# Optimization experiments

Measured on AMD Instinct MI355X. Metric: run time of the kernel, lower is better.

## Reference

```python
import jax, jax.numpy as jnp
import numpy as np

EPS = 1e-4  # clamp floor used by the torch module

def setup_inputs() -> dict:
    key = jax.random.key(0)
    k1, k2, k3, k4, k5 = jax.random.split(key, 5)
    B, C, T, BOT = 32, 1536, 2000, 128
    x = jax.random.normal(k1, (B, C, T), dtype=jnp.float32)
    W1 = jax.random.normal(k2, (BOT, 3 * C), dtype=jnp.float32) * 0.02
    b1 = jax.random.normal(k3, (BOT,), dtype=jnp.float32) * 0.02
    W2 = jax.random.normal(k4, (C, BOT), dtype=jnp.float32) * 0.02
    b2 = jax.random.normal(k5, (C,), dtype=jnp.float32) * 0.02
    return {"x": x, "W1": W1, "b1": b1, "W2": W2, "b2": b2}

def reference(x, W1, b1, W2, b2):
    # x: [B, C, T]
    T = x.shape[-1]
    mean = jnp.mean(x, axis=2, keepdims=True)                       # [B,C,1]
    var = jnp.var(x, axis=2, keepdims=True, ddof=1)                 # torch.var is unbiased
    std = jnp.sqrt(jnp.clip(var, EPS, None))                        # [B,C,1]
    glob = jnp.concatenate(
        [x,
         jnp.broadcast_to(mean, x.shape),
         jnp.broadcast_to(std, x.shape)], axis=1)                   # [B,3C,T]
    # conv1x1 -> relu -> conv1x1 over channel dim
    h = jnp.einsum('oc,bct->bot', W1, glob) + b1[None, :, None]     # [B,BOT,T]
    h = jax.nn.relu(h)
    w = jnp.einsum('ob,bkt->bot'.replace('bkt','xkt').replace('bot','xot'), W2, h)  # placeholder avoided
    w = jnp.einsum('cb,xbt->xct', W2, h) + b2[None, :, None]        # [B,C,T]
    w = jax.nn.softmax(w, axis=2)                                   # softmax over time
    wmean = jnp.sum(x * w, axis=2)                                  # [B,C]
    wsd = jnp.sqrt(jnp.clip(jnp.sum(x * x * w, axis=2) - wmean ** 2, EPS, None))
    return jnp.concatenate([wmean, wsd], axis=1)                    # [B,2C]
```

## Files before the change

kernel.cpp:

```cpp
#include <hip/hip_runtime.h>
#include <hip/hip_bf16.h>
#include <math.h>
#include <float.h>

#define B_    32
#define C_    1536
#define T_    2000
#define TP_   2048
#define BOT_  128
#define EPS_  1e-4f

#define CH    64
#define NCH   24
#define TC    128
#define NTS   16
#define NT_ST 8

typedef __attribute__((ext_vector_type(8))) short short8;
typedef __attribute__((ext_vector_type(4))) short short4v;
typedef __attribute__((ext_vector_type(4))) float f32x4;

static __device__ __forceinline__ unsigned short f2bf(float f) {
    unsigned u = __float_as_uint(f);
    u += 0x7FFFu + ((u >> 16) & 1u);
    return (unsigned short)(u >> 16);
}
static __device__ __forceinline__ float bf2f(unsigned short u) {
    return __uint_as_float(((unsigned)u) << 16);
}

__global__ __launch_bounds__(256) void stats_transpose(
    const float* __restrict__ x, float* __restrict__ spart,
    unsigned short* __restrict__ xt) {
    const int cb0 = blockIdx.x * 64;
    const int tc  = blockIdx.y;
    const int b   = blockIdx.z;
    const int tid = threadIdx.x;
    const int crow = tid >> 4;
    const int t4   = tid & 15;

    __shared__ __align__(16) unsigned short Tl[64 * 72];

    const float* xb = x + ((size_t)b * C_ + cb0) * T_;
    unsigned short* xo = xt + (size_t)b * TP_ * C_ + cb0;

    float s1[4] = {0.f, 0.f, 0.f, 0.f}, s2[4] = {0.f, 0.f, 0.f, 0.f};

    const int tt0 = tc * 256;
    for (int tt = tt0; tt < tt0 + 256; tt += 64) {
        __syncthreads();
        const int tg = tt + t4 * 4;
        #pragma unroll
        for (int i = 0; i < 4; ++i) {
            const int c = crow + 16 * i;
            f32x4 v;
            if (tg < T_) {
                v = *reinterpret_cast<const f32x4*>(xb + (size_t)c * T_ + tg);
            } else {
                v = (f32x4){0.f, 0.f, 0.f, 0.f};
            }
            s1[i] += (v[0] + v[1]) + (v[2] + v[3]);
            s2[i] = fmaf(v[0], v[0], fmaf(v[1], v[1],
                    fmaf(v[2], v[2], fmaf(v[3], v[3], s2[i]))));
            #pragma unroll
            for (int j = 0; j < 4; ++j)
                Tl[(t4 * 4 + j) * 72 + c] = f2bf(v[j]);
        }
        __syncthreads();
        #pragma unroll
        for (int jj = 0; jj < 2; ++jj) {
            int idx = tid + 256 * jj;
            int t = idx >> 3, c8 = idx & 7;
            short8 vv = *reinterpret_cast<const short8*>(&Tl[t * 72 + c8 * 8]);
            *reinterpret_cast<short8*>(xo + (size_t)(tt + t) * C_ + c8 * 8) = vv;
        }
    }

    #pragma unroll
    for (int i = 0; i < 4; ++i) {
        #pragma unroll
        for (int off = 1; off < 16; off <<= 1) {
            s1[i] += __shfl_xor(s1[i], off);
            s2[i] += __shfl_xor(s2[i], off);
        }
    }
    if (t4 == 0) {
        float* sp = spart + ((size_t)(b * NT_ST + tc) * 2) * C_ + cb0;
        #pragma unroll
        for (int i = 0; i < 4; ++i) {
            const int c = crow + 16 * i;
            sp[c]      = s1[i];
            sp[C_ + c] = s2[i];
        }
    }
}

__global__ __launch_bounds__(256) void cvt_kernel(
    const float* __restrict__ W1, const float* __restrict__ W2,
    unsigned short* __restrict__ W1b, unsigned short* __restrict__ W2b) {
    int idx = blockIdx.x * 256 + threadIdx.x;
    if (idx < BOT_ * C_) {
        int o = idx / C_, c = idx - o * C_;
        W1b[idx] = f2bf(W1[(size_t)o * (3 * C_) + c]);
        W2b[idx] = f2bf(W2[idx]);
    }
}

__global__ __launch_bounds__(256) void cb_kernel(
    const float* __restrict__ W1, const float* __restrict__ b1,
    const float* __restrict__ spart, float* __restrict__ cb) {
    __shared__ __align__(16) float ml[C_];
    __shared__ __align__(16) float sl[C_];
    const int b = blockIdx.x, tid = threadIdx.x;

    for (int c = tid; c < C_; c += 256) {
        float s1 = 0.f, s2 = 0.f;
        #pragma unroll
        for (int tc = 0; tc < NT_ST; ++tc) {
            const float* sp = spart + ((size_t)(b * NT_ST + tc) * 2) * C_ + c;
            s1 += sp[0];
            s2 += sp[C_];
        }
        float mean = s1 / (float)T_;
        float var  = (s2 - s1 * mean) / (float)(T_ - 1);
        ml[c] = mean;
        sl[c] = sqrtf(fmaxf(var, EPS_));
    }
    __syncthreads();

    const int grp = tid >> 4, j = tid & 15;
    #pragma unroll
    for (int p = 0; p < 8; ++p) {
        const int o = p * 16 + grp;
        const float* wm = W1 + (size_t)o * (3 * C_) + C_;
        const float* ws = wm + C_;
        float am = 0.f, as = 0.f;
        #pragma unroll 4
        for (int k = 0; k < 24; ++k) {
            const int c = k * 64 + j * 4;
            float4 wmv = *reinterpret_cast<const float4*>(wm + c);
            float4 wsv = *reinterpret_cast<const float4*>(ws + c);
            float4 mlv = *reinterpret_cast<const float4*>(&ml[c]);
            float4 slv = *reinterpret_cast<const float4*>(&sl[c]);
            am = fmaf(wmv.x, mlv.x, fmaf(wmv.y, mlv.y,
                 fmaf(wmv.z, mlv.z, fmaf(wmv.w, mlv.w, am))));
            as = fmaf(wsv.x, slv.x, fmaf(wsv.y, slv.y,
                 fmaf(wsv.z, slv.z, fmaf(wsv.w, slv.w, as))));
        }
        float v = am + as;
        v += __shfl_xor(v, 1); v += __shfl_xor(v, 2);
        v += __shfl_xor(v, 4); v += __shfl_xor(v, 8);
        if (j == 0) cb[(size_t)b * BOT_ + o] = b1[o] + v;
    }
}

typedef const __attribute__((address_space(1))) unsigned int* gas_ptr;
typedef __attribute__((address_space(3))) unsigned int* las_ptr;

__global__ __launch_bounds__(512) void fused_main(
    const unsigned short* __restrict__ xt,
    const unsigned short* __restrict__ W1b, const unsigned short* __restrict__ W2b,
    const float* __restrict__ cb, float* __restrict__ part) {
    const int b   = blockIdx.y;
    const int ts  = blockIdx.x;
    const int t0  = ts * TC;
    const int tid = threadIdx.x;
    const int lane = tid & 63;
    const int w   = tid >> 6;
    const int oh  = w >> 2, th = w & 3;
    const int g   = lane >> 4, li = lane & 15;

    __shared__ __align__(16) unsigned short LDS[4 * 8192];
    unsigned short* Hl = LDS;

    const unsigned short* xtb = xt + (size_t)b * TP_ * C_;

    f32x4 hacc[4][2];
    #pragma unroll
    for (int mi = 0; mi < 4; ++mi)
        #pragma unroll
        for (int ni = 0; ni < 2; ++ni)
            hacc[mi][ni] = (f32x4){0.f, 0.f, 0.f, 0.f};

    const unsigned short* gX[2];
    const unsigned short* gW[2];
    #pragma unroll
    for (int i = 0; i < 2; ++i) {
        int s = i * 512 + tid;
        int r = s >> 3, sl = s & 7;
        gX[i] = xtb + (size_t)(t0 + r) * C_ + ((sl ^ (r & 7)) * 8);
        gW[i] = W1b + (size_t)r * C_ + ((sl ^ (r & 7)) * 8);
    }

    auto STAGE = [&](int p, int kc) {
        unsigned short* bx = LDS + p * 16384;
        unsigned short* bw = bx + 8192;
        #pragma unroll
        for (int i = 0; i < 2; ++i)
            __builtin_amdgcn_global_load_lds(
                (gas_ptr)(gX[i] + kc), (las_ptr)&bx[(i * 512 + w * 64) * 8], 16, 0, 0);
        #pragma unroll
        for (int i = 0; i < 2; ++i)
            __builtin_amdgcn_global_load_lds(
                (gas_ptr)(gW[i] + kc), (las_ptr)&bw[(i * 512 + w * 64) * 8], 16, 0, 0);
    };

    auto COMPUTE = [&](int p) {
        const unsigned short* bx = LDS + p * 16384;
        const unsigned short* bw = bx + 8192;
        __builtin_amdgcn_s_setprio(1);
        #pragma unroll
        for (int ks = 0; ks < 2; ++ks) {
            short8 a[4], bb4[2];
            #pragma unroll
            for (int mi = 0; mi < 4; ++mi) {
                int o = oh * 64 + mi * 16 + li;
                a[mi] = *reinterpret_cast<const short8*>(
                    &bw[o * 64 + (((ks * 4 + g) ^ (o & 7)) << 3)]);
            }
            #pragma unroll
            for (int ni = 0; ni < 2; ++ni) {
                int t = th * 32 + ni * 16 + li;
                bb4[ni] = *reinterpret_cast<const short8*>(
                    &bx[t * 64 + (((ks * 4 + g) ^ (t & 7)) << 3)]);
            }
            #pragma unroll
            for (int mi = 0; mi < 4; ++mi)
                #pragma unroll
                for (int ni = 0; ni < 2; ++ni)
                    hacc[mi][ni] = __builtin_amdgcn_mfma_f32_16x16x32_bf16(a[mi], bb4[ni], hacc[mi][ni], 0, 0, 0);
        }
        __builtin_amdgcn_s_setprio(0);
    };

    STAGE(0, 0);
    STAGE(1, CH);

    for (int k = 0; k < NCH - 1; ++k) {
        const int cur = k & 1;
        asm volatile("s_waitcnt vmcnt(4)" ::: "memory");
        __builtin_amdgcn_s_barrier();
        COMPUTE(cur);
        __builtin_amdgcn_s_barrier();
        if (k + 2 < NCH) STAGE(cur, (k + 2) * CH);
    }
    asm volatile("s_waitcnt vmcnt(0)" ::: "memory");
    __builtin_amdgcn_s_barrier();
    COMPUTE((NCH - 1) & 1);

    __syncthreads();
    #pragma unroll
    for (int mi = 0; mi < 4; ++mi) {
        const int ob = oh * 64 + mi * 16 + g * 4;
        const float4 cbv = *reinterpret_cast<const float4*>(cb + (size_t)b * BOT_ + ob);
        const int so = ob >> 3, off = ob & 7;
        #pragma unroll
        for (int ni = 0; ni < 2; ++ni) {
            int t = th * 32 + ni * 16 + li;
            short4v pk;
            pk[0] = (short)f2bf(fmaxf(hacc[mi][ni][0] + cbv.x, 0.f));
            pk[1] = (short)f2bf(fmaxf(hacc[mi][ni][1] + cbv.y, 0.f));
            pk[2] = (short)f2bf(fmaxf(hacc[mi][ni][2] + cbv.z, 0.f));
            pk[3] = (short)f2bf(fmaxf(hacc[mi][ni][3] + cbv.w, 0.f));
            *reinterpret_cast<short4v*>(
                &Hl[t * 128 + ((so ^ (t & 7)) << 3) + off]) = pk;
        }
    }
    __syncthreads();

    float* pbase = part + ((size_t)(b * NTS + ts) * 3) * C_;

    for (int ccb = 0; ccb < C_; ccb += 128) {
        const int c = ccb + w * 16 + li;
        short8 bfr[4];
        #pragma unroll
        for (int ks = 0; ks < 4; ++ks)
            bfr[ks] = *reinterpret_cast<const short8*>(
                W2b + (size_t)c * BOT_ + ks * 32 + g * 8);

        float Z = 0.f, S1 = 0.f, S2 = 0.f;
        #pragma unroll
        for (int th2 = 0; th2 < 2; ++th2) {
            f32x4 lacc[4];
            #pragma unroll
            for (int ni = 0; ni < 4; ++ni) lacc[ni] = (f32x4){0.f, 0.f, 0.f, 0.f};
            __builtin_amdgcn_s_setprio(1);
            #pragma unroll
            for (int ks = 0; ks < 4; ++ks) {
                short8 af[4];
                #pragma unroll
                for (int ni = 0; ni < 4; ++ni) {
                    int t = th2 * 64 + ni * 16 + li;
                    af[ni] = *reinterpret_cast<const short8*>(
                        &Hl[t * 128 + (((ks * 4 + g) ^ (t & 7)) << 3)]);
                }
                #pragma unroll
                for (int ni = 0; ni < 4; ++ni)
                    lacc[ni] = __builtin_amdgcn_mfma_f32_16x16x32_bf16(af[ni], bfr[ks], lacc[ni], 0, 0, 0);
            }
            __builtin_amdgcn_s_setprio(0);
            #pragma unroll
            for (int ni = 0; ni < 4; ++ni)
                #pragma unroll
                for (int r = 0; r < 4; ++r) {
                    int tl = th2 * 64 + ni * 16 + g * 4 + r;
                    int t  = t0 + tl;
                    float p = __expf(lacc[ni][r]);
                    p = (t < T_) ? p : 0.f;
                    float xx = bf2f(xtb[(size_t)t * C_ + c]);
                    Z += p;
                    S1 = fmaf(xx, p, S1);
                    S2 = fmaf(xx * xx, p, S2);
                }
        }
        Z  += __shfl_xor(Z, 16);  Z  += __shfl_xor(Z, 32);
        S1 += __shfl_xor(S1, 16); S1 += __shfl_xor(S1, 32);
        S2 += __shfl_xor(S2, 16); S2 += __shfl_xor(S2, 32);
        if (lane < 16) {
            pbase[c]          = Z;
            pbase[C_ + c]     = S1;
            pbase[2 * C_ + c] = S2;
        }
    }
}

__global__ __launch_bounds__(256) void reduce_kernel(
    const float* __restrict__ part, float* __restrict__ out) {
    const int c = blockIdx.x * 256 + threadIdx.x;
    const int b = blockIdx.y;
    float Z = 0.f, S1 = 0.f, S2 = 0.f;
    for (int ts = 0; ts < NTS; ++ts) {
        const float* pb = part + ((size_t)(b * NTS + ts) * 3) * C_ + c;
        Z  += pb[0];
        S1 += pb[C_];
        S2 += pb[2 * C_];
    }
    float wmean = S1 / Z;
    float wsd   = sqrtf(fmaxf(S2 / Z - wmean * wmean, EPS_));
    out[(size_t)b * (2 * C_) + c]      = wmean;
    out[(size_t)b * (2 * C_) + C_ + c] = wsd;
}

extern "C" void kernel_launch(void* const* d_in, const int* in_sizes, int n_in,
                              void* d_out, int out_size, void* d_ws, size_t ws_size,
                              hipStream_t stream) {
    const float* x  = (const float*)d_in[0];
    const float* W1 = (const float*)d_in[1];
    const float* b1 = (const float*)d_in[2];
    const float* W2 = (const float*)d_in[3];
    float* out = (float*)d_out;

    float* ws = (float*)d_ws;
    float* cb     = ws;
    float* spart  = cb + (size_t)B_ * BOT_;
    float* part   = spart + (size_t)B_ * NT_ST * 2 * C_;
    unsigned short* W1b = (unsigned short*)(part + (size_t)B_ * NTS * 3 * C_);
    unsigned short* W2b = W1b + (size_t)BOT_ * C_;
    unsigned short* xt  = W2b + (size_t)C_ * BOT_;

    stats_transpose<<<dim3(C_ / 64, NT_ST, B_), 256, 0, stream>>>(x, spart, xt);
    cvt_kernel<<<dim3((BOT_ * C_ + 255) / 256), 256, 0, stream>>>(W1, W2, W1b, W2b);
    cb_kernel<<<dim3(B_), 256, 0, stream>>>(W1, b1, spart, cb);
    fused_main<<<dim3(NTS, B_), 512, 0, stream>>>(xt, W1b, W2b, cb, part);
    reduce_kernel<<<dim3(C_ / 256, B_), 256, 0, stream>>>(part, out);
}
```

Baseline: 270.6 us.

## Split X and W1 staging into a triple-buffered X and double-buffered W pipeline

The GEMM K-loop now stages the activation tile and the weight tile separately. Activation tiles get three LDS slots and are prefetched three chunks ahead, while weight tiles keep two slots and are fetched only one chunk ahead. The idea is to hide the DRAM-bound activation loads better, on the assumption that the weights, shared across batches, stay hot in L2. The cost is a larger LDS footprint and only a short latency window for each weight load, which could stall if the weights miss in cache.

Result: no change. 274.7 us (+1.5%).

```diff
diff --git a/kernel.cpp b/kernel.cpp
--- a/kernel.cpp
+++ b/kernel.cpp
@@ -170,7 +170,7 @@
     const int oh  = w >> 2, th = w & 3;
     const int g   = lane >> 4, li = lane & 15;
 
-    __shared__ __align__(16) unsigned short LDS[4 * 8192];
+    __shared__ __align__(16) unsigned short LDS[5 * 8192];
     unsigned short* Hl = LDS;
 
     const unsigned short* xtb = xt + (size_t)b * TP_ * C_;
@@ -192,22 +192,24 @@
         gW[i] = W1b + (size_t)r * C_ + ((sl ^ (r & 7)) * 8);
     }
 
-    auto STAGE = [&](int p, int kc) {
-        unsigned short* bx = LDS + p * 16384;
-        unsigned short* bw = bx + 8192;
+    auto STAGE_X = [&](int slot, int kc) {
+        unsigned short* bx = LDS + slot * 8192;
         #pragma unroll
         for (int i = 0; i < 2; ++i)
             __builtin_amdgcn_global_load_lds(
                 (gas_ptr)(gX[i] + kc), (las_ptr)&bx[(i * 512 + w * 64) * 8], 16, 0, 0);
+    };
+    auto STAGE_W = [&](int slot, int kc) {
+        unsigned short* bw = LDS + (3 + slot) * 8192;
         #pragma unroll
         for (int i = 0; i < 2; ++i)
             __builtin_amdgcn_global_load_lds(
                 (gas_ptr)(gW[i] + kc), (las_ptr)&bw[(i * 512 + w * 64) * 8], 16, 0, 0);
     };
 
-    auto COMPUTE = [&](int p) {
-        const unsigned short* bx = LDS + p * 16384;
-        const unsigned short* bw = bx + 8192;
+    auto COMPUTE = [&](int xs, int wsl) {
+        const unsigned short* bx = LDS + xs * 8192;
+        const unsigned short* bw = LDS + (3 + wsl) * 8192;
         __builtin_amdgcn_s_setprio(1);
         #pragma unroll
         for (int ks = 0; ks < 2; ++ks) {
@@ -233,20 +235,26 @@
         __builtin_amdgcn_s_setprio(0);
     };
 
-    STAGE(0, 0);
-    STAGE(1, CH);
-
-    for (int k = 0; k < NCH - 1; ++k) {
-        const int cur = k & 1;
-        asm volatile("s_waitcnt vmcnt(4)" ::: "memory");
+    STAGE_X(0, 0);
+    STAGE_X(1, CH);
+    STAGE_W(0, 0);
+    STAGE_X(2, 2 * CH);
+
+    int xs = 0, wsl = 0;
+    for (int k = 0; k < NCH; ++k) {
+        if (k < NCH - 2) {
+            asm volatile("s_waitcnt vmcnt(2)" ::: "memory");
+        } else {
+            asm volatile("s_waitcnt vmcnt(0)" ::: "memory");
+        }
         __builtin_amdgcn_s_barrier();
-        COMPUTE(cur);
+        COMPUTE(xs, wsl);
         __builtin_amdgcn_s_barrier();
-        if (k + 2 < NCH) STAGE(cur, (k + 2) * CH);
-    }
-    asm volatile("s_waitcnt vmcnt(0)" ::: "memory");
-    __builtin_amdgcn_s_barrier();
-    COMPUTE((NCH - 1) & 1);
+        if (k + 1 < NCH) STAGE_W(wsl ^ 1, (k + 1) * CH);
+        if (k + 3 < NCH) STAGE_X(xs, (k + 3) * CH);
+        xs  = (xs == 2) ? 0 : xs + 1;
+        wsl = wsl ^ 1;
+    }
 
     __syncthreads();
     #pragma unroll
```

## Fold weight conversion into stats kernel and bias computation into main kernel

Applied to the files above, without the earlier changes.

The bf16 weight conversion now runs as an extra grid slice of the stats/transpose kernel, and the per-batch constant bias (W1 mean/std terms) is computed at the start of each fused_main block into shared memory. Together these remove two kernel launches and the global cb round-trip. In exchange, every one of the 16 time-slice blocks per batch recomputes the same 128x3072 dot products, which adds redundant W1 reads and a prologue before the GEMM pipeline starts.

Measured after the change: 361.9 us. 1.34x slower.

```diff
diff --git a/kernel.cpp b/kernel.cpp
--- a/kernel.cpp
+++ b/kernel.cpp
@@ -31,11 +31,22 @@
 
 __global__ __launch_bounds__(256) void stats_transpose(
     const float* __restrict__ x, float* __restrict__ spart,
-    unsigned short* __restrict__ xt) {
-    const int cb0 = blockIdx.x * 64;
+    unsigned short* __restrict__ xt,
+    const float* __restrict__ W1, const float* __restrict__ W2,
+    unsigned short* __restrict__ W1b, unsigned short* __restrict__ W2b) {
     const int tc  = blockIdx.y;
     const int b   = blockIdx.z;
     const int tid = threadIdx.x;
+
+    if (tc == NT_ST) {
+        int base = (b * (C_ / 64) + blockIdx.x) * 256 + tid;
+        int o = base / C_, c = base - o * C_;
+        W1b[base] = f2bf(W1[(size_t)o * (3 * C_) + c]);
+        W2b[base] = f2bf(W2[base]);
+        return;
+    }
+
+    const int cb0 = blockIdx.x * 64;
     const int crow = tid >> 4;
     const int t4   = tid & 15;
 
@@ -95,72 +106,14 @@
     }
 }
 
-__global__ __launch_bounds__(256) void cvt_kernel(
-    const float* __restrict__ W1, const float* __restrict__ W2,
-    unsigned short* __restrict__ W1b, unsigned short* __restrict__ W2b) {
-    int idx = blockIdx.x * 256 + threadIdx.x;
-    if (idx < BOT_ * C_) {
-        int o = idx / C_, c = idx - o * C_;
-        W1b[idx] = f2bf(W1[(size_t)o * (3 * C_) + c]);
-        W2b[idx] = f2bf(W2[idx]);
-    }
-}
-
-__global__ __launch_bounds__(256) void cb_kernel(
-    const float* __restrict__ W1, const float* __restrict__ b1,
-    const float* __restrict__ spart, float* __restrict__ cb) {
-    __shared__ __align__(16) float ml[C_];
-    __shared__ __align__(16) float sl[C_];
-    const int b = blockIdx.x, tid = threadIdx.x;
-
-    for (int c = tid; c < C_; c += 256) {
-        float s1 = 0.f, s2 = 0.f;
-        #pragma unroll
-        for (int tc = 0; tc < NT_ST; ++tc) {
-            const float* sp = spart + ((size_t)(b * NT_ST + tc) * 2) * C_ + c;
-            s1 += sp[0];
-            s2 += sp[C_];
-        }
-        float mean = s1 / (float)T_;
-        float var  = (s2 - s1 * mean) / (float)(T_ - 1);
-        ml[c] = mean;
-        sl[c] = sqrtf(fmaxf(var, EPS_));
-    }
-    __syncthreads();
-
-    const int grp = tid >> 4, j = tid & 15;
-    #pragma unroll
-    for (int p = 0; p < 8; ++p) {
-        const int o = p * 16 + grp;
-        const float* wm = W1 + (size_t)o * (3 * C_) + C_;
-        const float* ws = wm + C_;
-        float am = 0.f, as = 0.f;
-        #pragma unroll 4
-        for (int k = 0; k < 24; ++k) {
-            const int c = k * 64 + j * 4;
-            float4 wmv = *reinterpret_cast<const float4*>(wm + c);
-            float4 wsv = *reinterpret_cast<const float4*>(ws + c);
-            float4 mlv = *reinterpret_cast<const float4*>(&ml[c]);
-            float4 slv = *reinterpret_cast<const float4*>(&sl[c]);
-            am = fmaf(wmv.x, mlv.x, fmaf(wmv.y, mlv.y,
-                 fmaf(wmv.z, mlv.z, fmaf(wmv.w, mlv.w, am))));
-            as = fmaf(wsv.x, slv.x, fmaf(wsv.y, slv.y,
-                 fmaf(wsv.z, slv.z, fmaf(wsv.w, slv.w, as))));
-        }
-        float v = am + as;
-        v += __shfl_xor(v, 1); v += __shfl_xor(v, 2);
-        v += __shfl_xor(v, 4); v += __shfl_xor(v, 8);
-        if (j == 0) cb[(size_t)b * BOT_ + o] = b1[o] + v;
-    }
-}
-
 typedef const __attribute__((address_space(1))) unsigned int* gas_ptr;
 typedef __attribute__((address_space(3))) unsigned int* las_ptr;
 
 __global__ __launch_bounds__(512) void fused_main(
     const unsigned short* __restrict__ xt,
     const unsigned short* __restrict__ W1b, const unsigned short* __restrict__ W2b,
-    const float* __restrict__ cb, float* __restrict__ part) {
+    const float* __restrict__ W1, const float* __restrict__ b1,
+    const float* __restrict__ spart, float* __restrict__ part) {
     const int b   = blockIdx.y;
     const int ts  = blockIdx.x;
     const int t0  = ts * TC;
@@ -170,10 +123,51 @@
     const int oh  = w >> 2, th = w & 3;
     const int g   = lane >> 4, li = lane & 15;
 
-    __shared__ __align__(16) unsigned short LDS[4 * 8192];
+    __shared__ __align__(16) unsigned short LDS[4 * 8192 + 256];
     unsigned short* Hl = LDS;
+    float* cbl = reinterpret_cast<float*>(LDS + 4 * 8192);
 
     const unsigned short* xtb = xt + (size_t)b * TP_ * C_;
+
+    {
+        float* mlp = reinterpret_cast<float*>(LDS);
+        float* slp = mlp + C_;
+        for (int c = tid; c < C_; c += 512) {
+            float s1 = 0.f, s2 = 0.f;
+            #pragma unroll
+            for (int tc = 0; tc < NT_ST; ++tc) {
+                const float* sp = spart + ((size_t)(b * NT_ST + tc) * 2) * C_ + c;
+                s1 += sp[0];
+                s2 += sp[C_];
+            }
+            float mean = s1 / (float)T_;
+            float var  = (s2 - s1 * mean) / (float)(T_ - 1);
+            mlp[c] = mean;
+            slp[c] = sqrtf(fmaxf(var, EPS_));
+        }
+        __syncthreads();
+        const int o = tid >> 2, q = tid & 3;
+        const float* wm = W1 + (size_t)o * (3 * C_) + C_;
+        const float* ws = wm + C_;
+        float am = 0.f, as = 0.f;
+        const int c0 = q * 384;
+        #pragma unroll 4
+        for (int k = 0; k < 96; ++k) {
+            const int c = c0 + k * 4;
+            float4 wmv = *reinterpret_cast<const float4*>(wm + c);
+            float4 wsv = *reinterpret_cast<const float4*>(ws + c);
+            float4 mlv = *reinterpret_cast<const float4*>(&mlp[c]);
+            float4 slv = *reinterpret_cast<const float4*>(&slp[c]);
+            am = fmaf(wmv.x, mlv.x, fmaf(wmv.y, mlv.y,
+                 fmaf(wmv.z, mlv.z, fmaf(wmv.w, mlv.w, am))));
+            as = fmaf(wsv.x, slv.x, fmaf(wsv.y, slv.y,
+                 fmaf(wsv.z, slv.z, fmaf(wsv.w, slv.w, as))));
+        }
+        float v = am + as;
+        v += __shfl_xor(v, 1); v += __shfl_xor(v, 2);
+        if (q == 0) cbl[o] = b1[o] + v;
+        __syncthreads();
+    }
 
     f32x4 hacc[4][2];
     #pragma unroll
@@ -252,7 +246,7 @@
     #pragma unroll
     for (int mi = 0; mi < 4; ++mi) {
         const int ob = oh * 64 + mi * 16 + g * 4;
-        const float4 cbv = *reinterpret_cast<const float4*>(cb + (size_t)b * BOT_ + ob);
+        const float4 cbv = *reinterpret_cast<const float4*>(&cbl[ob]);
         const int so = ob >> 3, off = ob & 7;
         #pragma unroll
         for (int ni = 0; ni < 2; ++ni) {
@@ -351,16 +345,15 @@
     float* out = (float*)d_out;
 
     float* ws = (float*)d_ws;
-    float* cb     = ws;
-    float* spart  = cb + (size_t)B_ * BOT_;
+    float* spart  = ws;
     float* part   = spart + (size_t)B_ * NT_ST * 2 * C_;
     unsigned short* W1b = (unsigned short*)(part + (size_t)B_ * NTS * 3 * C_);
     unsigned short* W2b = W1b + (size_t)BOT_ * C_;
     unsigned short* xt  = W2b + (size_t)C_ * BOT_;
 
-    stats_transpose<<<dim3(C_ / 64, NT_ST, B_), 256, 0, stream>>>(x, spart, xt);
-    cvt_kernel<<<dim3((BOT_ * C_ + 255) / 256), 256, 0, stream>>>(W1, W2, W1b, W2b);
-    cb_kernel<<<dim3(B_), 256, 0, stream>>>(W1, b1, spart, cb);
-    fused_main<<<dim3(NTS, B_), 512, 0, stream>>>(xt, W1b, W2b, cb, part);
+    stats_transpose<<<dim3(C_ / 64, NT_ST + 1, B_), 256, 0, stream>>>(
+        x, spart, xt, W1, W2, W1b, W2b);
+    fused_main<<<dim3(NTS, B_), 512, 0, stream>>>(
+        xt, W1b, W2b, W1, b1, spart, part);
     reduce_kernel<<<dim3(C_ / 256, B_), 256, 0, stream>>>(part, out);
 }
```
